# Kernel optimization log

Hardware: AMD Instinct MI355X
Metric: run time of the kernel (lower is better)

## Reference

```python
import jax, jax.numpy as jnp
import numpy as np

T, B, L, F, H = 32, 32, 128, 512, 1024
SCALE = 1.0 / np.sqrt(float(L))  # 1/sqrt(max_demonstration_length)


def _lstm_step(h, c, x, W_ih, W_hh, b_ih, b_hh):
    # PyTorch LSTM gate order: i, f, g, o
    gates = x @ W_ih.T + b_ih + h @ W_hh.T + b_hh
    i, f, g, o = jnp.split(gates, 4, axis=-1)
    c = jax.nn.sigmoid(f) * c + jax.nn.sigmoid(i) * jnp.tanh(g)
    h = jax.nn.sigmoid(o) * jnp.tanh(c)
    return h, c


def setup_inputs() -> dict:
    key = jax.random.key(0)
    ks = jax.random.split(key, 20)
    s = 0.02
    d = {
        'demonstration': jax.random.normal(ks[0], (T, B, L, F), jnp.float32),
        'demonstration_lengths': jax.random.randint(ks[1], (B,), 0, L),
        'current_obs': jax.random.normal(ks[2], (T, B, F), jnp.float32),
        'h0': jnp.zeros((1, B, H), jnp.float32),
        'c0': jnp.zeros((1, B, H), jnp.float32),
        # demonstration_encoder LSTM(F -> H)
        'enc_W_ih': jax.random.normal(ks[3], (4 * H, F), jnp.float32) * s,
        'enc_W_hh': jax.random.normal(ks[4], (4 * H, H), jnp.float32) * s,
        'enc_b_ih': jnp.zeros((4 * H,), jnp.float32),
        'enc_b_hh': jnp.zeros((4 * H,), jnp.float32),
        # attn Linear(H -> H)
        'attn_W': jax.random.normal(ks[5], (H, H), jnp.float32) * s,
        'attn_b': jnp.zeros((H,), jnp.float32),
        # attn_combine MLP: (F + H) -> 4H -> H
        'mlp_W1': jax.random.normal(ks[6], (4 * H, F + H), jnp.float32) * s,
        'mlp_b1': jnp.zeros((4 * H,), jnp.float32),
        'mlp_W2': jax.random.normal(ks[7], (H, 4 * H), jnp.float32) * s,
        'mlp_b2': jnp.zeros((H,), jnp.float32),
        # recurrent LSTM(H -> H)
        'lstm_W_ih': jax.random.normal(ks[8], (4 * H, H), jnp.float32) * s,
        'lstm_W_hh': jax.random.normal(ks[9], (4 * H, H), jnp.float32) * s,
        'lstm_b_ih': jnp.zeros((4 * H,), jnp.float32),
        'lstm_b_hh': jnp.zeros((4 * H,), jnp.float32),
    }
    return d


def reference(demonstration, demonstration_lengths, current_obs, h0, c0,
              enc_W_ih, enc_W_hh, enc_b_ih, enc_b_hh,
              attn_W, attn_b, mlp_W1, mlp_b1, mlp_W2, mlp_b2,
              lstm_W_ih, lstm_W_hh, lstm_b_ih, lstm_b_hh):
    # Encode demonstration[0] (B, L, F) with an LSTM over the L axis.
    x_demo = jnp.transpose(demonstration[0], (1, 0, 2))  # (L, B, F)

    def enc(carry, xt):
        h, c = carry
        h, c = _lstm_step(h, c, xt, enc_W_ih, enc_W_hh, enc_b_ih, enc_b_hh)
        return (h, c), h

    z0 = jnp.zeros((B, H), demonstration.dtype)
    _, demo_enc = jax.lax.scan(enc, (z0, z0), x_demo)  # (L, B, H)
    demo_enc = jnp.transpose(demo_enc, (1, 0, 2))       # (B, L, H)

    # attn(demo_enc) is t-invariant; hoist it out of the loop (same math).
    attn_proj = demo_enc @ attn_W.T + attn_b            # (B, L, H)

    mask = (jnp.arange(L)[None, :] < demonstration_lengths[:, None])
    mask = mask.at[:, 0].set(True)                      # (B, L)

    def step(carry, obs_t):
        h, c = carry  # (B, H)
        scores = jnp.einsum('blh,bh->bl', attn_proj, h) * SCALE
        scores = jnp.where(mask, scores, -jnp.inf)
        w = jax.nn.softmax(scores, axis=-1)             # (B, L)
        ctx = jnp.einsum('bl,blh->bh', w, demo_enc)     # (B, H)
        z = jnp.concatenate([ctx, obs_t], axis=-1)      # (B, H+F)
        m = jax.nn.relu(z @ mlp_W1.T + mlp_b1)          # MLP hidden relu
        x = jax.nn.relu(m @ mlp_W2.T + mlp_b2)          # outer relu in forward
        h, c = _lstm_step(h, c, x, lstm_W_ih, lstm_W_hh, lstm_b_ih, lstm_b_hh)
        return (h, c), h

    (hT, cT), q = jax.lax.scan(step, (h0[0], c0[0]), current_obs)
    return q, hT[None], cT[None]
```

## Files before the change

### kernel.cpp

```cpp
#include <hip/hip_runtime.h>

typedef unsigned short u16;
typedef unsigned int   u32;
typedef short s8v __attribute__((ext_vector_type(8)));
typedef float f4v __attribute__((ext_vector_type(4)));

#define TT 32
#define BB 32
#define LL 128
#define FF 512
#define HH 1024
#define G4 4096
#define SCALE_ 0.08838834764831845f

__device__ __forceinline__ u16 f2bf(float f){
  u32 u = __float_as_uint(f);
  u32 r = u + 0x7fffu + ((u >> 16) & 1u);
  return (u16)(r >> 16);
}
__device__ __forceinline__ float bf2f(u16 s){ return __uint_as_float(((u32)s) << 16); }
__device__ __forceinline__ float sigf(float x){ return 1.f / (1.f + __expf(-x)); }

__device__ __forceinline__ void mfma16(f4v& d, s8v a, s8v b){
  asm("v_mfma_f32_16x16x32_bf16 %0, %1, %2, %0" : "+v"(d) : "v"(a), "v"(b));
}

typedef __attribute__((address_space(3))) u32 as3u32;
typedef __attribute__((address_space(1))) u32 as1u32;
__device__ __forceinline__ void glds16(const u16* g, u16* l){
  __builtin_amdgcn_global_load_lds((const as1u32*)g, (as3u32*)l, 16, 0, 0);
}

__device__ __forceinline__ void stcc_u16(u16* p, u16 v){
  u32 vv = v;
  asm volatile("global_store_short %0, %1, off sc0 sc1" :: "v"(p), "v"(vv) : "memory");
}
__device__ __forceinline__ void stcc_f32(float* p, float v){
  asm volatile("global_store_dword %0, %1, off sc0 sc1" :: "v"(p), "v"(v) : "memory");
}
__device__ __forceinline__ u32 poll_ld(const u32* p){
  u32 v;
  asm volatile("global_load_dword %0, %1, off sc0 sc1\n\ts_waitcnt vmcnt(0)"
               : "=v"(v) : "v"(p) : "memory");
  return v;
}

__device__ __forceinline__ void gbar(u32* cnt, u32 nblk, u32& epoch){
  asm volatile("s_waitcnt vmcnt(0)" ::: "memory");
  __syncthreads();
  ++epoch;
  if (threadIdx.x == 0){
    atomicAdd(cnt, 1u);
    u32 target = epoch * nblk;
    while (poll_ld(cnt) < target) __builtin_amdgcn_s_sleep(1);
  }
  __syncthreads();
}

__device__ __forceinline__ void stg_issue(const u16* __restrict__ src, s8v* tmp, int rstride){
  const int tid = threadIdx.x;
  const int row = tid >> 5, s0 = tid & 31;
  const u16* p = src + (size_t)row * rstride + s0 * 8;
  #pragma unroll
  for (int i = 0; i < 4; i++) tmp[i] = *(const s8v*)(p + i * 256);
}
__device__ __forceinline__ void stg_commit(const s8v* tmp, u16* lds){
  const int tid = threadIdx.x;
  const int row = tid >> 5, s0 = tid & 31;
  char* base = (char*)lds + (row << 11);
  u32 x = (u32)(row & 15) << 4;
  #pragma unroll
  for (int i = 0; i < 4; i++){
    u32 cb = (u32)(s0 + 32 * i) << 4;
    *(s8v*)(base + (cb ^ x)) = tmp[i];
  }
}
__device__ __forceinline__ void st5_issue(const u16* __restrict__ src, s8v* tmp, int rstride){
  const int tid = threadIdx.x;
  const int row = tid >> 4, s0 = tid & 15;
  const u16* p = src + (size_t)row * rstride + s0 * 8;
  #pragma unroll
  for (int i = 0; i < 8; i++) tmp[i] = *(const s8v*)(p + i * 128);
}
__device__ __forceinline__ void st5_commit(const s8v* tmp, u16* lds){
  const int tid = threadIdx.x;
  const int row = tid >> 4, s0 = tid & 15;
  char* base = (char*)lds + (row << 11);
  u32 x = (u32)(row & 15) << 4;
  #pragma unroll
  for (int i = 0; i < 8; i++){
    u32 cb = (u32)(s0 + 16 * i) << 4;
    *(s8v*)(base + (cb ^ x)) = tmp[i];
  }
}
__device__ __forceinline__ void st16_issue(const u16* __restrict__ src, s8v* tmp, int rstride){
  const int tid = threadIdx.x;
  const int row = tid >> 5, s0 = tid & 31;
  const u16* p = src + (size_t)row * rstride + s0 * 8;
  #pragma unroll
  for (int i = 0; i < 4; i++) tmp[i] = *(const s8v*)(p + i * 256);
}
__device__ __forceinline__ void st16_commit(const s8v* tmp, u16* lds){
  const int tid = threadIdx.x;
  const int row = tid >> 5, s0 = tid & 31;
  char* base = (char*)lds + (row << 11);
  u32 x = (u32)(row & 15) << 4;
  #pragma unroll
  for (int i = 0; i < 4; i++){
    u32 cb = (u32)(s0 + 32 * i) << 4;
    *(s8v*)(base + (cb ^ x)) = tmp[i];
  }
}
__device__ __forceinline__ s8v ldsA(const u16* lds, int row, int cb){
  return *(const s8v*)((const char*)lds + (row << 11) + (cb ^ ((row & 15) << 4)));
}

__global__ void k_convert(const float* __restrict__ src, u16* __restrict__ dst, int n){
  int i = blockIdx.x * blockDim.x + threadIdx.x;
  int st = gridDim.x * blockDim.x;
  for (; i < n; i += st) dst[i] = f2bf(src[i]);
}
__global__ void k_split_w1(const float* __restrict__ w1, u16* __restrict__ w1c, u16* __restrict__ w1o){
  int i = blockIdx.x * blockDim.x + threadIdx.x;
  int st = gridDim.x * blockDim.x;
  const int n = G4 * (FF + HH);
  for (; i < n; i += st){
    int j = i / 1536, k = i - j * 1536;
    u16 v = f2bf(w1[i]);
    if (k < HH) w1c[j * HH + k] = v;
    else        w1o[j * FF + (k - HH)] = v;
  }
}
__global__ void k_addb(const float* __restrict__ a, const float* __restrict__ b,
                       float* __restrict__ o, int n){
  int i = blockIdx.x * blockDim.x + threadIdx.x;
  int st = gridDim.x * blockDim.x;
  for (; i < n; i += st) o[i] = a[i] + b[i];
}
__global__ void k_demo_t(const float* __restrict__ d, u16* __restrict__ o){
  const int n = LL * BB * FF;
  int i = blockIdx.x * blockDim.x + threadIdx.x;
  int st = gridDim.x * blockDim.x;
  for (; i < n; i += st){
    int f = i & 511;
    int row = i >> 9;
    int l = row >> 5, b = row & 31;
    o[i] = f2bf(d[(size_t)b * (LL * FF) + l * FF + f]);
  }
}

template<int RELU>
__global__ void __launch_bounds__(256) k_gemm_bt(const u16* __restrict__ A, const u16* __restrict__ B,
        const float* __restrict__ bias, u16* __restrict__ C, int M, int N, int K)
{
  __shared__ u16 As[128 * 64];
  __shared__ u16 Bs[128 * 64];
  const int tid = threadIdx.x;
  const int lane = tid & 63, wave = tid >> 6;
  const int m0 = blockIdx.x * 128, n0 = blockIdx.y * 128;
  const int wm = wave >> 1, wn = wave & 1;
  const int lr = lane & 15, lk = (lane >> 4) * 8;
  f4v acc[4][4];
  #pragma unroll
  for (int i = 0; i < 4; i++)
    #pragma unroll
    for (int j = 0; j < 4; j++) acc[i][j] = f4v{0.f, 0.f, 0.f, 0.f};

  for (int kt = 0; kt < K; kt += 64){
    #pragma unroll
    for (int i = 0; i < 4; i++){
      int c = tid + i * 256;
      int row = c >> 3, cc = (c & 7) * 8;
      glds16(A + (size_t)(m0 + row) * K + kt + cc, &As[c * 8]);
      glds16(B + (size_t)(n0 + row) * K + kt + cc, &Bs[c * 8]);
    }
    __syncthreads();
    #pragma unroll
    for (int ks = 0; ks < 2; ++ks){
      int ko = ks * 32 + lk;
      s8v av[4], bv[4];
      #pragma unroll
      for (int m = 0; m < 4; m++) av[m] = *(const s8v*)&As[(wm * 64 + m * 16 + lr) * 64 + ko];
      #pragma unroll
      for (int n = 0; n < 4; n++) bv[n] = *(const s8v*)&Bs[(wn * 64 + n * 16 + lr) * 64 + ko];
      #pragma unroll
      for (int m = 0; m < 4; m++)
        #pragma unroll
        for (int n = 0; n < 4; n++) mfma16(acc[m][n], av[m], bv[n]);
    }
    __syncthreads();
  }
  const int r0 = (lane >> 4) * 4;
  #pragma unroll
  for (int m = 0; m < 4; m++){
    #pragma unroll
    for (int n = 0; n < 4; n++){
      int col = n0 + wn * 64 + n * 16 + lr;
      float bc = bias[col];
      #pragma unroll
      for (int r = 0; r < 4; r++){
        int row = m0 + wm * 64 + m * 16 + r0 + r;
        float v = acc[m][n][r] + bc;
        if (RELU) v = fmaxf(v, 0.f);
        C[(size_t)row * N + col] = f2bf(v);
      }
    }
  }
}

union SMemE { u16 stage[32768]; float gx[16][32][17]; };

__global__ void __launch_bounds__(1024, 4) k_encoder(const u16* __restrict__ Whh, const u16* __restrict__ Xih,
      u16* __restrict__ zslot, u16* __restrict__ denc, u32* bar)
{
  __shared__ SMemE sm;
  const int nb = blockIdx.x, tid = threadIdx.x;
  const int lane = tid & 63, w = tid >> 6;
  const int jc = nb * 16;
  const int lr = lane & 15, lk = (lane >> 4) * 8;
  const int eb = tid >> 4, ejj = tid & 15;
  const int rb = (lane >> 4) * 4;

  if (tid < 512) stcc_u16(&zslot[eb * HH + jc + ejj], 0);
  float cr = 0.f;
  u32 epoch = 0;
  gbar(bar, 64, epoch);

  const int kh = (w & 3) * 256;
  const u16* Wb = Whh + (size_t)((w >> 2) * HH + jc + lr) * HH + kh + lk;
  for (int l = 0; l < LL; ++l){
    const u16* hb = (l == 0) ? zslot : (denc + (size_t)(l - 1) * (BB * HH));
    s8v ht[4];
    stg_issue(hb, ht, HH);
    float xi = 0, xf = 0, xg = 0, xo = 0;
    if (tid < 512){
      const u16* xr = Xih + ((size_t)(l * BB + eb)) * G4 + jc + ejj;
      xi = bf2f(xr[0]); xf = bf2f(xr[1024]); xg = bf2f(xr[2048]); xo = bf2f(xr[3072]);
    }
    stg_commit(ht, sm.stage);
    __syncthreads();
    f4v a0 = {0.f,0.f,0.f,0.f}, a1 = {0.f,0.f,0.f,0.f};
    #pragma unroll
    for (int ks = 0; ks < 8; ++ks){
      int cb = (kh + lk + ks * 32) * 2;
      s8v va0 = ldsA(sm.stage, lr,      cb);
      s8v va1 = ldsA(sm.stage, lr + 16, cb);
      s8v vb  = *(const s8v*)(Wb + ks * 32);
      mfma16(a0, va0, vb);
      mfma16(a1, va1, vb);
    }
    __syncthreads();
    #pragma unroll
    for (int r = 0; r < 4; r++){ sm.gx[w][rb + r][lr] = a0[r]; sm.gx[w][16 + rb + r][lr] = a1[r]; }
    __syncthreads();
    if (tid < 512){
      float gi = sm.gx[0][eb][ejj] + sm.gx[1][eb][ejj] + sm.gx[2][eb][ejj] + sm.gx[3][eb][ejj] + xi;
      float gf = sm.gx[4][eb][ejj] + sm.gx[5][eb][ejj] + sm.gx[6][eb][ejj] + sm.gx[7][eb][ejj] + xf;
      float gg = sm.gx[8][eb][ejj] + sm.gx[9][eb][ejj] + sm.gx[10][eb][ejj] + sm.gx[11][eb][ejj] + xg;
      float go = sm.gx[12][eb][ejj] + sm.gx[13][eb][ejj] + sm.gx[14][eb][ejj] + sm.gx[15][eb][ejj] + xo;
      cr = sigf(gf) * cr + sigf(gi) * tanhf(gg);
      float h = sigf(go) * tanhf(cr);
      stcc_u16(&denc[(size_t)l * (BB * HH) + eb * HH + jc + ejj], f2bf(h));
    }
    gbar(bar, 64, epoch);
  }
}

union SMemD {
  u16 stage[32768];
  float gx[8][32][17];
  struct { float swt[128]; } a;
  char pad[98304];
};

__global__ void __launch_bounds__(512, 1) k_decoder(
    const u16* __restrict__ aproj, const u16* __restrict__ denc, const u16* __restrict__ obsp,
    const u16* __restrict__ W1c, const u16* __restrict__ W2w, const u16* __restrict__ WihL,
    const u16* __restrict__ WhhL, const float* __restrict__ blstm, const float* __restrict__ b2,
    const float* __restrict__ h0, const float* __restrict__ c0, const int* __restrict__ lens,
    float* __restrict__ hfR, u16* __restrict__ hbR, u16* __restrict__ ctxR,
    u16* __restrict__ mbR, u16* __restrict__ xbR, float* __restrict__ scX,
    float* __restrict__ out, u32* bar)
{
  __shared__ SMemD sm;
  const int p = blockIdx.x;
  const int nb = (p & 7) * 16 + (p >> 3);
  const int tid = threadIdx.x;
  const int lane = tid & 63, w = tid >> 6;
  const int lr = lane & 15, lk = (lane >> 4) * 8;
  const int rb = (lane >> 4) * 4;
  const int eb = tid >> 4, ejj = tid & 15;
  const int ab = nb & 31, aq = nb >> 5;
  const int pb = nb >> 1, bh = nb & 1;
  const int jc = pb * 16;

  float cr = 0.f;
  if (tid < 256){
    int b = bh * 16 + (tid >> 4), col = jc + (tid & 15);
    float hv = h0[b * HH + col];
    stcc_f32(&hfR[b * HH + col], hv);
    stcc_u16(&hbR[b * HH + col], f2bf(hv));
    cr = c0[b * HH + col];
  }
  u32 epoch = 0;
  gbar(bar, 128, epoch);

  for (int t = 0; t < TT; ++t){
    const u16* ctxS = ctxR + (size_t)t * (BB * HH);
    const u16* mbS  = mbR  + (size_t)t * (BB * G4);
    const u16* xbS  = xbR  + (size_t)t * (BB * HH);
    const u16* hbS  = hbR  + (size_t)t * (BB * HH);
    const float* hfS= hfR  + (size_t)t * (BB * HH);
    float* scT = scX + (size_t)t * (BB * 128) + ab * 128;

    {
      const int len = lens[ab];
      float hr[16];
      const float* hp = hfS + ab * HH + lane * 16;
      #pragma unroll
      for (int i = 0; i < 16; i++) hr[i] = hp[i];
      #pragma unroll
      for (int i = 0; i < 4; ++i){
        int l = aq * 32 + w * 4 + i;
        const u16* ap = aproj + ((size_t)(l * BB + ab)) * HH + lane * 16;
        s8v v0 = *(const s8v*)ap;
        s8v v1 = *(const s8v*)(ap + 8);
        float s = 0.f;
        #pragma unroll
        for (int k = 0; k < 8; k++) s += bf2f((u16)v0[k]) * hr[k];
        #pragma unroll
        for (int k = 0; k < 8; k++) s += bf2f((u16)v1[k]) * hr[8 + k];
        #pragma unroll
        for (int off = 32; off > 0; off >>= 1) s += __shfl_down(s, off);
        if (lane == 0){
          s *= SCALE_;
          if (l >= len && l != 0) s = -__builtin_inff();
          stcc_f32(&scT[l], s);
        }
      }
    }
    gbar(bar, 128, epoch);

    {
      if (w == 0){
        float x0 = scT[lane], x1 = scT[lane + 64];
        float mx = fmaxf(x0, x1);
        #pragma unroll
        for (int off = 32; off > 0; off >>= 1) mx = fmaxf(mx, __shfl_xor(mx, off));
        float e0 = __expf(x0 - mx), e1 = __expf(x1 - mx);
        float smv = e0 + e1;
        #pragma unroll
        for (int off = 32; off > 0; off >>= 1) smv += __shfl_xor(smv, off);
        float inv = 1.f / smv;
        sm.a.swt[lane] = e0 * inv;
        sm.a.swt[lane + 64] = e1 * inv;
      }
      __syncthreads();
      if (tid < 256){
        int col = aq * 256 + tid;
        const u16* dp = denc + (size_t)ab * HH + col;
        float acc = 0.f;
        #pragma unroll 4
        for (int l = 0; l < LL; ++l)
          acc += sm.a.swt[l] * bf2f(dp[(size_t)l * (BB * HH)]);
        stcc_u16((u16*)&ctxS[ab * HH + col], f2bf(acc));
      }
    }
    gbar(bar, 128, epoch);

    {
      s8v ct[8];
      st5_issue(ctxS, ct, HH);
      st5_commit(ct, sm.stage);
      __syncthreads();
      const int col0 = nb * 32 + (w >> 2) * 16;
      const int kh = (w & 3) * 256;
      f4v a0 = {0.f,0.f,0.f,0.f}, a1 = {0.f,0.f,0.f,0.f};
      const u16* Bp = W1c + (size_t)(col0 + lr) * HH + kh + lk;
      #pragma unroll
      for (int ks = 0; ks < 8; ++ks){
        int cb = (kh + lk + ks * 32) * 2;
        s8v va0 = ldsA(sm.stage, lr,      cb);
        s8v va1 = ldsA(sm.stage, lr + 16, cb);
        s8v vb  = *(const s8v*)(Bp + ks * 32);
        mfma16(a0, va0, vb);
        mfma16(a1, va1, vb);
      }
      __syncthreads();
      #pragma unroll
      for (int r = 0; r < 4; r++){ sm.gx[w][rb + r][lr] = a0[r]; sm.gx[w][16 + rb + r][lr] = a1[r]; }
      __syncthreads();
      #pragma unroll
      for (int cg = 0; cg < 2; ++cg){
        int col = nb * 32 + cg * 16 + ejj;
        float v = sm.gx[4 * cg][eb][ejj] + sm.gx[4 * cg + 1][eb][ejj]
                + sm.gx[4 * cg + 2][eb][ejj] + sm.gx[4 * cg + 3][eb][ejj]
                + bf2f(obsp[((size_t)(t * BB + eb)) * G4 + col]);
        stcc_u16((u16*)&mbS[eb * G4 + col], f2bf(fmaxf(v, 0.f)));
      }
    }
    gbar(bar, 128, epoch);

    {
      f4v a0 = {0.f,0.f,0.f,0.f};
      for (int q = 0; q < 4; ++q){
        s8v ct[4];
        st16_issue(mbS + (size_t)(bh * 16) * G4 + q * 1024, ct, G4);
        st16_commit(ct, sm.stage);
        __syncthreads();
        const u16* Bp = W2w + (size_t)(jc + lr) * G4 + q * 1024 + w * 128 + lk;
        #pragma unroll
        for (int ks = 0; ks < 4; ++ks){
          int cb = (w * 128 + lk + ks * 32) * 2;
          s8v va0 = ldsA(sm.stage, lr, cb);
          s8v vb  = *(const s8v*)(Bp + ks * 32);
          mfma16(a0, va0, vb);
        }
        __syncthreads();
      }
      #pragma unroll
      for (int r = 0; r < 4; r++) sm.gx[w][rb + r][lr] = a0[r];
      __syncthreads();
      if (tid < 256){
        int bb = tid >> 4, cc = tid & 15;
        float v = b2[jc + cc];
        #pragma unroll
        for (int g = 0; g < 8; ++g) v += sm.gx[g][bb][cc];
        stcc_u16((u16*)&xbS[(bh * 16 + bb) * HH + jc + cc], f2bf(fmaxf(v, 0.f)));
      }
    }
    gbar(bar, 128, epoch);

    {
      s8v xt[4], ht[4];
      st16_issue(xbS + (size_t)(bh * 16) * HH, xt, HH);
      st16_issue(hbS + (size_t)(bh * 16) * HH, ht, HH);
      st16_commit(xt, sm.stage);
      st16_commit(ht, sm.stage + 16384);
      __syncthreads();
      const int gate = w >> 1, kh = (w & 1) * 512;
      f4v a0 = {0.f,0.f,0.f,0.f};
      const u16* Bx = WihL + (size_t)(gate * HH + jc + lr) * HH + kh + lk;
      #pragma unroll
      for (int ks = 0; ks < 16; ++ks){
        int cb = (kh + lk + ks * 32) * 2;
        mfma16(a0, ldsA(sm.stage, lr, cb), *(const s8v*)(Bx + ks * 32));
      }
      const u16* Bh = WhhL + (size_t)(gate * HH + jc + lr) * HH + kh + lk;
      #pragma unroll
      for (int ks = 0; ks < 16; ++ks){
        int cb = (kh + lk + ks * 32) * 2;
        mfma16(a0, ldsA(sm.stage + 16384, lr, cb), *(const s8v*)(Bh + ks * 32));
      }
      __syncthreads();
      #pragma unroll
      for (int r = 0; r < 4; r++) sm.gx[w][rb + r][lr] = a0[r];
      __syncthreads();
      if (tid < 256){
        int bb = tid >> 4, cc = tid & 15;
        int b = bh * 16 + bb, col = jc + cc;
        float gi = sm.gx[0][bb][cc] + sm.gx[1][bb][cc] + blstm[col];
        float gf = sm.gx[2][bb][cc] + sm.gx[3][bb][cc] + blstm[1024 + col];
        float gg = sm.gx[4][bb][cc] + sm.gx[5][bb][cc] + blstm[2048 + col];
        float go = sm.gx[6][bb][cc] + sm.gx[7][bb][cc] + blstm[3072 + col];
        cr = sigf(gf) * cr + sigf(gi) * tanhf(gg);
        float h = sigf(go) * tanhf(cr);
        stcc_f32(&out[(size_t)t * (BB * HH) + b * HH + col], h);
        stcc_f32(&hfR[(size_t)(t + 1) * (BB * HH) + b * HH + col], h);
        stcc_u16(&hbR[(size_t)(t + 1) * (BB * HH) + b * HH + col], f2bf(h));
        if (t == TT - 1){
          stcc_f32(&out[1048576 + b * HH + col], h);
          stcc_f32(&out[1081344 + b * HH + col], cr);
        }
      }
    }
    gbar(bar, 128, epoch);
  }
}

static constexpr size_t oWihE = 0;
static constexpr size_t oWhhE = oWihE + 4194304;
static constexpr size_t oAttnW= oWhhE + 8388608;
static constexpr size_t oW1C  = oAttnW+ 2097152;
static constexpr size_t oW1O  = oW1C  + 8388608;
static constexpr size_t oW2   = oW1O  + 4194304;
static constexpr size_t oWihL = oW2   + 8388608;
static constexpr size_t oWhhL = oWihL + 8388608;
static constexpr size_t oBEnc = oWhhL + 8388608;
static constexpr size_t oBL   = oBEnc + 16384;
static constexpr size_t oDemoT= oBL   + 16384;
static constexpr size_t oObsB = oDemoT+ 4194304;
static constexpr size_t oXih  = oObsB + 1048576;
static constexpr size_t oObsP = oXih  + 33554432;
static constexpr size_t oDEnc = oObsP + 8388608;
static constexpr size_t oAPrj = oDEnc + 8388608;
static constexpr size_t oZE   = oAPrj + 8388608;
static constexpr size_t oHFR  = oZE   + 65536;
static constexpr size_t oHBR  = oHFR  + 4325376;
static constexpr size_t oCtxR = oHBR  + 2162688;
static constexpr size_t oMBR  = oCtxR + 2097152;
static constexpr size_t oXBR  = oMBR  + 8388608;
static constexpr size_t oScX  = oXBR  + 2097152;
static constexpr size_t oBar  = oScX  + 524288;

extern "C" void kernel_launch(void* const* d_in, const int* in_sizes, int n_in,
                              void* d_out, int out_size, void* d_ws, size_t ws_size,
                              hipStream_t stream)
{
  const float* demo = (const float*)d_in[0];
  const int*   lens = (const int*)  d_in[1];
  const float* obs  = (const float*)d_in[2];
  const float* h0   = (const float*)d_in[3];
  const float* c0   = (const float*)d_in[4];
  const float* eWih = (const float*)d_in[5];
  const float* eWhh = (const float*)d_in[6];
  const float* eBih = (const float*)d_in[7];
  const float* eBhh = (const float*)d_in[8];
  const float* aW   = (const float*)d_in[9];
  const float* aB   = (const float*)d_in[10];
  const float* W1   = (const float*)d_in[11];
  const float* B1   = (const float*)d_in[12];
  const float* W2   = (const float*)d_in[13];
  const float* B2   = (const float*)d_in[14];
  const float* lWih = (const float*)d_in[15];
  const float* lWhh = (const float*)d_in[16];
  const float* lBih = (const float*)d_in[17];
  const float* lBhh = (const float*)d_in[18];

  char* ws = (char*)d_ws;
  u16*  WihE = (u16*)(ws + oWihE);
  u16*  WhhE = (u16*)(ws + oWhhE);
  u16*  AttnW= (u16*)(ws + oAttnW);
  u16*  W1C  = (u16*)(ws + oW1C);
  u16*  W1O  = (u16*)(ws + oW1O);
  u16*  W2w  = (u16*)(ws + oW2);
  u16*  WihL = (u16*)(ws + oWihL);
  u16*  WhhL = (u16*)(ws + oWhhL);
  float* BEnc= (float*)(ws + oBEnc);
  float* BL  = (float*)(ws + oBL);
  u16*  DemoT= (u16*)(ws + oDemoT);
  u16*  ObsB = (u16*)(ws + oObsB);
  u16*  Xih  = (u16*)(ws + oXih);
  u16*  ObsP = (u16*)(ws + oObsP);
  u16*  DEnc = (u16*)(ws + oDEnc);
  u16*  APrj = (u16*)(ws + oAPrj);
  u16*  ZE   = (u16*)(ws + oZE);
  float* HFR = (float*)(ws + oHFR);
  u16*  HBR  = (u16*)(ws + oHBR);
  u16*  CtxR = (u16*)(ws + oCtxR);
  u16*  MBR  = (u16*)(ws + oMBR);
  u16*  XBR  = (u16*)(ws + oXBR);
  float* ScX = (float*)(ws + oScX);
  u32*  Bar  = (u32*)(ws + oBar);

  k_convert<<<1024, 256, 0, stream>>>(eWih, WihE, G4 * FF);
  k_convert<<<1024, 256, 0, stream>>>(eWhh, WhhE, G4 * HH);
  k_convert<<<512,  256, 0, stream>>>(aW,   AttnW, HH * HH);
  k_split_w1<<<1024, 256, 0, stream>>>(W1, W1C, W1O);
  k_convert<<<1024, 256, 0, stream>>>(W2,   W2w,  HH * G4);
  k_convert<<<1024, 256, 0, stream>>>(lWih, WihL, G4 * HH);
  k_convert<<<1024, 256, 0, stream>>>(lWhh, WhhL, G4 * HH);
  k_addb<<<16, 256, 0, stream>>>(eBih, eBhh, BEnc, G4);
  k_addb<<<16, 256, 0, stream>>>(lBih, lBhh, BL, G4);
  k_demo_t<<<1024, 256, 0, stream>>>(demo, DemoT);
  k_convert<<<512, 256, 0, stream>>>(obs, ObsB, TT * BB * FF);
  hipMemsetAsync(Bar, 0, 256, stream);

  {
    dim3 g(LL * BB / 128, G4 / 128);
    k_gemm_bt<0><<<g, 256, 0, stream>>>(DemoT, WihE, BEnc, Xih, LL * BB, G4, FF);
  }
  {
    dim3 g(TT * BB / 128, G4 / 128);
    k_gemm_bt<0><<<g, 256, 0, stream>>>(ObsB, W1O, B1, ObsP, TT * BB, G4, FF);
  }

  k_encoder<<<64, 1024, 0, stream>>>(WhhE, Xih, ZE, DEnc, Bar);

  {
    dim3 g(LL * BB / 128, HH / 128);
    k_gemm_bt<0><<<g, 256, 0, stream>>>(DEnc, AttnW, aB, APrj, LL * BB, HH, HH);
  }

  k_decoder<<<128, 512, 0, stream>>>(APrj, DEnc, ObsP, W1C, W2w, WihL, WhhL,
                                     BL, B2, h0, c0, lens,
                                     HFR, HBR, CtxR, MBR, XBR, ScX,
                                     (float*)d_out, Bar + 16);
}
```

Measured before the change: 2.551 ms.

## Fuse attention phases per batch and overlap recurrent Whh GEMM with attention

Each of 32 blocks now computes scores, softmax and context for one batch row entirely in shared memory, which removes one grid-wide barrier per timestep. Blocks 32-95 concurrently compute h@Whh for the LSTM and write the partial gates to a new bf16 workspace, which the final LSTM phase reads back in place of recomputing them. The tradeoff is a longer serial attention phase on fewer blocks, an extra bf16 rounding of the Whh partial gates, and extra global traffic for the partial-gate buffer.

```diff
diff --git a/kernel.cpp b/kernel.cpp
--- a/kernel.cpp
+++ b/kernel.cpp
@@ -34,6 +34,9 @@
 __device__ __forceinline__ void stcc_u16(u16* p, u16 v){
   u32 vv = v;
   asm volatile("global_store_short %0, %1, off sc0 sc1" :: "v"(p), "v"(vv) : "memory");
+}
+__device__ __forceinline__ void stcc_u32(void* p, u32 v){
+  asm volatile("global_store_dword %0, %1, off sc0 sc1" :: "v"(p), "v"(v) : "memory");
 }
 __device__ __forceinline__ void stcc_f32(float* p, float v){
   asm volatile("global_store_dword %0, %1, off sc0 sc1" :: "v"(p), "v"(v) : "memory");
@@ -269,7 +272,7 @@
 union SMemD {
   u16 stage[32768];
   float gx[8][32][17];
-  struct { float swt[128]; } a;
+  struct { float ssc[128]; float swt[128]; } a;
   char pad[98304];
 };
 
@@ -279,7 +282,7 @@
     const u16* __restrict__ WhhL, const float* __restrict__ blstm, const float* __restrict__ b2,
     const float* __restrict__ h0, const float* __restrict__ c0, const int* __restrict__ lens,
     float* __restrict__ hfR, u16* __restrict__ hbR, u16* __restrict__ ctxR,
-    u16* __restrict__ mbR, u16* __restrict__ xbR, float* __restrict__ scX,
+    u16* __restrict__ mbR, u16* __restrict__ xbR, u16* __restrict__ pGh,
     float* __restrict__ out, u32* bar)
 {
   __shared__ SMemD sm;
@@ -290,7 +293,6 @@
   const int lr = lane & 15, lk = (lane >> 4) * 8;
   const int rb = (lane >> 4) * 4;
   const int eb = tid >> 4, ejj = tid & 15;
-  const int ab = nb & 31, aq = nb >> 5;
   const int pb = nb >> 1, bh = nb & 1;
   const int jc = pb * 16;
 
@@ -311,17 +313,17 @@
     const u16* xbS  = xbR  + (size_t)t * (BB * HH);
     const u16* hbS  = hbR  + (size_t)t * (BB * HH);
     const float* hfS= hfR  + (size_t)t * (BB * HH);
-    float* scT = scX + (size_t)t * (BB * 128) + ab * 128;
-
-    {
+    u16* pGhT = pGh + (size_t)t * (BB * G4);
+
+    if (p < 32){
+      const int ab = p;
       const int len = lens[ab];
       float hr[16];
       const float* hp = hfS + ab * HH + lane * 16;
       #pragma unroll
       for (int i = 0; i < 16; i++) hr[i] = hp[i];
-      #pragma unroll
-      for (int i = 0; i < 4; ++i){
-        int l = aq * 32 + w * 4 + i;
+      for (int i = 0; i < 16; ++i){
+        int l = w * 16 + i;
         const u16* ap = aproj + ((size_t)(l * BB + ab)) * HH + lane * 16;
         s8v v0 = *(const s8v*)ap;
         s8v v1 = *(const s8v*)(ap + 8);
@@ -335,15 +337,12 @@
         if (lane == 0){
           s *= SCALE_;
           if (l >= len && l != 0) s = -__builtin_inff();
-          stcc_f32(&scT[l], s);
+          sm.a.ssc[l] = s;
         }
       }
-    }
-    gbar(bar, 128, epoch);
-
-    {
+      __syncthreads();
       if (w == 0){
-        float x0 = scT[lane], x1 = scT[lane + 64];
+        float x0 = sm.a.ssc[lane], x1 = sm.a.ssc[lane + 64];
         float mx = fmaxf(x0, x1);
         #pragma unroll
         for (int off = 32; off > 0; off >>= 1) mx = fmaxf(mx, __shfl_xor(mx, off));
@@ -356,14 +355,49 @@
         sm.a.swt[lane + 64] = e1 * inv;
       }
       __syncthreads();
-      if (tid < 256){
-        int col = aq * 256 + tid;
+      {
+        int col = tid * 2;
         const u16* dp = denc + (size_t)ab * HH + col;
-        float acc = 0.f;
+        float a0 = 0.f, a1 = 0.f;
         #pragma unroll 4
-        for (int l = 0; l < LL; ++l)
-          acc += sm.a.swt[l] * bf2f(dp[(size_t)l * (BB * HH)]);
-        stcc_u16((u16*)&ctxS[ab * HH + col], f2bf(acc));
+        for (int l = 0; l < LL; ++l){
+          u32 dv = *(const u32*)(dp + (size_t)l * (BB * HH));
+          a0 += sm.a.swt[l] * bf2f((u16)(dv & 0xffff));
+          a1 += sm.a.swt[l] * bf2f((u16)(dv >> 16));
+        }
+        u32 pk = ((u32)f2bf(a1) << 16) | f2bf(a0);
+        stcc_u32((void*)(ctxS + ab * HH + col), pk);
+      }
+    } else if (p < 96){
+      const int gr = p - 32;
+      const int rows0 = gr * 64;
+      s8v ht[8];
+      st5_issue(hbS, ht, HH);
+      st5_commit(ht, sm.stage);
+      __syncthreads();
+      const int tile = w & 3, kh2 = (w >> 2) * 512;
+      f4v a0 = {0.f,0.f,0.f,0.f}, a1 = {0.f,0.f,0.f,0.f};
+      const u16* Bh = WhhL + (size_t)(rows0 + tile * 16 + lr) * HH + kh2 + lk;
+      #pragma unroll
+      for (int ks = 0; ks < 16; ++ks){
+        int cb = (kh2 + lk + ks * 32) * 2;
+        s8v va0 = ldsA(sm.stage, lr,      cb);
+        s8v va1 = ldsA(sm.stage, lr + 16, cb);
+        s8v vb  = *(const s8v*)(Bh + ks * 32);
+        mfma16(a0, va0, vb);
+        mfma16(a1, va1, vb);
+      }
+      __syncthreads();
+      #pragma unroll
+      for (int r = 0; r < 4; r++){ sm.gx[w][rb + r][lr] = a0[r]; sm.gx[w][16 + rb + r][lr] = a1[r]; }
+      __syncthreads();
+      {
+        int b = tid >> 4, rl = tid & 15;
+        #pragma unroll
+        for (int t2 = 0; t2 < 4; ++t2){
+          float v = sm.gx[t2][b][rl] + sm.gx[t2 + 4][b][rl];
+          stcc_u16(&pGhT[(size_t)b * G4 + rows0 + t2 * 16 + rl], f2bf(v));
+        }
       }
     }
     gbar(bar, 128, epoch);
@@ -432,11 +466,9 @@
     gbar(bar, 128, epoch);
 
     {
-      s8v xt[4], ht[4];
+      s8v xt[4];
       st16_issue(xbS + (size_t)(bh * 16) * HH, xt, HH);
-      st16_issue(hbS + (size_t)(bh * 16) * HH, ht, HH);
       st16_commit(xt, sm.stage);
-      st16_commit(ht, sm.stage + 16384);
       __syncthreads();
       const int gate = w >> 1, kh = (w & 1) * 512;
       f4v a0 = {0.f,0.f,0.f,0.f};
@@ -446,12 +478,6 @@
         int cb = (kh + lk + ks * 32) * 2;
         mfma16(a0, ldsA(sm.stage, lr, cb), *(const s8v*)(Bx + ks * 32));
       }
-      const u16* Bh = WhhL + (size_t)(gate * HH + jc + lr) * HH + kh + lk;
-      #pragma unroll
-      for (int ks = 0; ks < 16; ++ks){
-        int cb = (kh + lk + ks * 32) * 2;
-        mfma16(a0, ldsA(sm.stage + 16384, lr, cb), *(const s8v*)(Bh + ks * 32));
-      }
       __syncthreads();
       #pragma unroll
       for (int r = 0; r < 4; r++) sm.gx[w][rb + r][lr] = a0[r];
@@ -459,10 +485,11 @@
       if (tid < 256){
         int bb = tid >> 4, cc = tid & 15;
         int b = bh * 16 + bb, col = jc + cc;
-        float gi = sm.gx[0][bb][cc] + sm.gx[1][bb][cc] + blstm[col];
-        float gf = sm.gx[2][bb][cc] + sm.gx[3][bb][cc] + blstm[1024 + col];
-        float gg = sm.gx[4][bb][cc] + sm.gx[5][bb][cc] + blstm[2048 + col];
-        float go = sm.gx[6][bb][cc] + sm.gx[7][bb][cc] + blstm[3072 + col];
+        const u16* pg = pGhT + (size_t)b * G4 + col;
+        float gi = sm.gx[0][bb][cc] + sm.gx[1][bb][cc] + bf2f(pg[0])    + blstm[col];
+        float gf = sm.gx[2][bb][cc] + sm.gx[3][bb][cc] + bf2f(pg[1024]) + blstm[1024 + col];
+        float gg = sm.gx[4][bb][cc] + sm.gx[5][bb][cc] + bf2f(pg[2048]) + blstm[2048 + col];
+        float go = sm.gx[6][bb][cc] + sm.gx[7][bb][cc] + bf2f(pg[3072]) + blstm[3072 + col];
         cr = sigf(gf) * cr + sigf(gi) * tanhf(gg);
         float h = sigf(go) * tanhf(cr);
         stcc_f32(&out[(size_t)t * (BB * HH) + b * HH + col], h);
@@ -500,8 +527,8 @@
 static constexpr size_t oCtxR = oHBR  + 2162688;
 static constexpr size_t oMBR  = oCtxR + 2097152;
 static constexpr size_t oXBR  = oMBR  + 8388608;
-static constexpr size_t oScX  = oXBR  + 2097152;
-static constexpr size_t oBar  = oScX  + 524288;
+static constexpr size_t oPGh  = oXBR  + 2097152;
+static constexpr size_t oBar  = oPGh  + 8388608;
 
 extern "C" void kernel_launch(void* const* d_in, const int* in_sizes, int n_in,
                               void* d_out, int out_size, void* d_ws, size_t ws_size,
@@ -550,7 +577,7 @@
   u16*  CtxR = (u16*)(ws + oCtxR);
   u16*  MBR  = (u16*)(ws + oMBR);
   u16*  XBR  = (u16*)(ws + oXBR);
-  float* ScX = (float*)(ws + oScX);
+  u16*  PGh  = (u16*)(ws + oPGh);
   u32*  Bar  = (u32*)(ws + oBar);
 
   k_convert<<<1024, 256, 0, stream>>>(eWih, WihE, G4 * FF);
@@ -584,6 +611,6 @@
 
   k_decoder<<<128, 512, 0, stream>>>(APrj, DEnc, ObsP, W1C, W2w, WihL, WhhL,
                                      BL, B2, h0, c0, lens,
-                                     HFR, HBR, CtxR, MBR, XBR, ScX,
+                                     HFR, HBR, CtxR, MBR, XBR, PGh,
                                      (float*)d_out, Bar + 16);
 }
```

New measurement: 2.536 ms. About the same (-0.6%).
